# Optimization experiments

Measured on AMD Instinct MI355X. Metric: run time of the kernel, lower is better.

The kernel has to match this reference:

```python
import jax, jax.numpy as jnp
import numpy as np

CHAINS = [[15, 14, 13], [10, 11, 12], [5, 4, 3], [0, 1, 2]]
B, H, I = 2048, 1024, 3


def setup_inputs() -> dict:
    key = jax.random.key(0)
    ks = jax.random.split(key, 8)
    s = 1.0 / np.sqrt(H)
    return {
        "p3d": jax.random.normal(ks[0], (B, 16, I), dtype=jnp.float32),
        "Wih": jax.random.uniform(ks[1], (4 * H, I), jnp.float32, -s, s),
        "Whh": jax.random.uniform(ks[2], (4 * H, H), jnp.float32, -s, s),
        "bih": jax.random.uniform(ks[3], (4 * H,), jnp.float32, -s, s),
        "bhh": jax.random.uniform(ks[4], (4 * H,), jnp.float32, -s, s),
        "Wref": jax.random.uniform(ks[5], (I, H), jnp.float32, -s, s),
        "bref": jax.random.uniform(ks[6], (I,), jnp.float32, -s, s),
    }


def reference(p3d, Wih, Whh, bih, bhh, Wref, bref):
    # p3d: [B, 16, 3]; shared LSTMCell traverses the skeleton tree fwd+back.
    def cell(x, h, c):
        gates = x @ Wih.T + bih + h @ Whh.T + bhh  # [B, 4H]
        i, f, g, o = jnp.split(gates, 4, axis=-1)  # torch gate order i,f,g,o
        c2 = jax.nn.sigmoid(f) * c + jax.nn.sigmoid(i) * jnp.tanh(g)
        return jax.nn.sigmoid(o) * jnp.tanh(c2), c2

    z = jnp.zeros((p3d.shape[0], Whh.shape[1]), p3d.dtype)
    fh, fc = {}, {}
    # forward pass along limb chains (root of each chain starts from zeros)
    for chain in CHAINS:
        h, c = cell(p3d[:, chain[0]], z, z)
        fh[chain[0]], fc[chain[0]] = h, c
        for prev, cur in zip(chain[:-1], chain[1:]):
            h, c = cell(p3d[:, cur], fh[prev], fc[prev])
            fh[cur], fc[cur] = h, c
    # spine: merge hip ends (joints 2, 3) -> 6 -> 7
    hx, cx = (fh[2] + fh[3]) / 2, (fc[2] + fc[3]) / 2
    fh[6], fc[6] = cell(p3d[:, 6], hx, cx)
    fh[7], fc[7] = cell(p3d[:, 7], fh[6], fc[6])
    # merge neck + wrist ends (joints 7, 13, 12) -> 8 -> 9
    hx = (fh[7] + fh[13] + fh[12]) / 3
    cx = (fc[7] + fc[13] + fc[12]) / 3
    fh[8], fc[8] = cell(p3d[:, 8], hx, cx)
    fh[9], fc[9] = cell(p3d[:, 9], fh[8], fc[8])

    bh, bc = {}, {}
    bh[9], bc[9] = cell(p3d[:, 9], z, z)
    hx, cx = bh[9], bc[9]
    for i in [8, 7, 6]:
        hx, cx = cell(p3d[:, i], hx, cx)
        bh[i], bc[i] = hx, cx
    for chain in CHAINS:
        if chain[2] > 9:
            hx, cx = bh[8], bc[8]
        else:
            hx, cx = bh[6], bc[6]
        for i in reversed(chain):
            hx, cx = cell(p3d[:, i], hx, cx)
            bh[i], bc[i] = hx, cx

    FH = jnp.stack([fh[j] for j in range(16)], axis=1)  # [B, 16, H]
    BH = jnp.stack([bh[j] for j in range(16)], axis=1)  # [B, 16, H]
    out = (FH + BH) / 2.0
    return out @ Wref.T + bref  # [B, 16, 3]
```

## Files before the change

### kernel.cpp

```cpp
#include <hip/hip_runtime.h>
#include <cmath>

#define Bsz 2048
#define Hsz 1024
#define NG  4096
#define BM  256
#define BN  256
#define BK  64
#define NKT 16

typedef __attribute__((ext_vector_type(8))) short bf16x8;
typedef __attribute__((ext_vector_type(4))) float f32x4;

struct CellArgs {
  int ncells, b0;
  int joint[8];
  const short* hih[8];
  const float* cin[8];
  short* hoh[8];
  short* hol[8];
  float* cout[8];
};

struct ProjArgs {
  int ncells, b0;
  int joint[8];
  const short* hh[8];
  const short* hl[8];
};

__device__ __forceinline__ float sigmoidf_(float x) {
  return 1.0f / (1.0f + __expf(-x));
}
__device__ __forceinline__ float fast_tanh(float x) {
  float ax = fabsf(x);
  float e = __expf(2.0f * ax);
  float t = 1.0f - 2.0f / (e + 1.0f);
  return copysignf(t, x);
}
__device__ __forceinline__ float bf2f(short b) {
  unsigned u = ((unsigned)(unsigned short)b) << 16;
  float f; __builtin_memcpy(&f, &u, 4); return f;
}
__device__ __forceinline__ short f2bf(float f) {
  unsigned u; __builtin_memcpy(&u, &f, 4);
  u += 0x7fffu + ((u >> 16) & 1u);
  return (short)(u >> 16);
}
__device__ __forceinline__ void gl_lds16(const void* g, void* l) {
  __builtin_amdgcn_global_load_lds(
      (const __attribute__((address_space(1))) unsigned int*)g,
      (__attribute__((address_space(3))) unsigned int*)l, 16, 0, 0);
}

__launch_bounds__(512, 2)
__global__ void cell_kernel(const float* __restrict__ p3d,
                            const short* __restrict__ Whi,
                            const float4* __restrict__ wb,
                            CellArgs A) {
  __shared__ short Atile[2][BM * BK];
  __shared__ short Btile[2][BN * BK];
  __shared__ float xs[BM * 4];

  const int z = blockIdx.z;
  const short* __restrict__ hih = A.hih[z];
  const float* __restrict__ cin = A.cin[z];
  short* __restrict__ hoh = A.hoh[z];
  short* __restrict__ hol = A.hol[z];
  float* __restrict__ co  = A.cout[z];

  const int t = threadIdx.x;
  const int lane = t & 63;
  const int w = t >> 6;
  const int wm = w >> 2;
  const int wn = w & 3;
  const int m0 = blockIdx.x * BM;
  const int hc0 = blockIdx.y * 64;
  const int lc = lane & 15;
  const int kg = lane >> 4;
  const int xorv = lc & 7;

  const int l8 = lane >> 3, l7 = lane & 7;
  const int sSlot = (l7 ^ (l8 & 7)) * 8;
  int aOff[4], bOff[4];
  #pragma unroll
  for (int j = 0; j < 4; ++j) {
    const int chunk = j * 8 + w;
    aOff[j] = (m0 + chunk * 8 + l8) * Hsz + sSlot;
    const int np = chunk * 8 + l8;
    const int g = (np >> 4) & 3;
    const int hcl = ((np >> 6) << 4) + (np & 15);
    bOff[j] = (g * Hsz + hc0 + hcl) * Hsz + sSlot;
  }

  if (t < BM) {
    const float* p = p3d + ((size_t)(A.b0 + m0 + t) * 16 + A.joint[z]) * 3;
    xs[t * 4 + 0] = p[0];
    xs[t * 4 + 1] = p[1];
    xs[t * 4 + 2] = p[2];
  }
  __syncthreads();

  f32x4 acc[8][4];
  #pragma unroll
  for (int mf = 0; mf < 8; ++mf)
    #pragma unroll
    for (int nf = 0; nf < 4; ++nf) acc[mf][nf] = (f32x4){0.f, 0.f, 0.f, 0.f};

  const bool hasH = (hih != nullptr);

  auto stage = [&](int kt, int p) {
    const int k0 = kt * BK;
    #pragma unroll
    for (int j = 0; j < 4; ++j)
      gl_lds16(hih + aOff[j] + k0, &Atile[p][(j * 8 + w) * 512]);
    #pragma unroll
    for (int j = 0; j < 4; ++j)
      gl_lds16(Whi + bOff[j] + k0, &Btile[p][(j * 8 + w) * 512]);
  };

  if (hasH) {
    stage(0, 0);
    stage(1, 1);
    asm volatile("s_waitcnt vmcnt(8)" ::: "memory");
    __builtin_amdgcn_s_barrier();

    for (int kt = 0; kt < NKT; ++kt) {
      const int p = kt & 1;
      const short* Ab = &Atile[p][0];
      const short* Bb = &Btile[p][0];
      #pragma unroll
      for (int ks = 0; ks < 2; ++ks) {
        bf16x8 af[8], bf[4];
        #pragma unroll
        for (int mf = 0; mf < 8; ++mf) {
          const int r = wm * 128 + mf * 16 + lc;
          af[mf] = *(const bf16x8*)(Ab + r * 64 + (((ks * 4 + kg) ^ xorv) * 8));
        }
        #pragma unroll
        for (int nf = 0; nf < 4; ++nf) {
          const int np = wn * 64 + nf * 16 + lc;
          bf[nf] = *(const bf16x8*)(Bb + np * 64 + (((ks * 4 + kg) ^ xorv) * 8));
        }
        __builtin_amdgcn_s_setprio(1);
        #pragma unroll
        for (int mf = 0; mf < 8; ++mf)
          #pragma unroll
          for (int nf = 0; nf < 4; ++nf)
            acc[mf][nf] = __builtin_amdgcn_mfma_f32_16x16x32_bf16(
                af[mf], bf[nf], acc[mf][nf], 0, 0, 0);
        __builtin_amdgcn_s_setprio(0);
      }
      asm volatile("s_waitcnt lgkmcnt(0)" ::: "memory");
      __builtin_amdgcn_s_barrier();
      if (kt + 2 < NKT) {
        stage(kt + 2, p);
        asm volatile("s_waitcnt vmcnt(8)" ::: "memory");
      } else {
        asm volatile("s_waitcnt vmcnt(0)" ::: "memory");
      }
      __builtin_amdgcn_s_barrier();
    }
  }

  const int hc = hc0 + wn * 16 + lc;
  float4 wv[4];
  #pragma unroll
  for (int g = 0; g < 4; ++g) wv[g] = wb[g * Hsz + hc];
  #pragma unroll
  for (int mf = 0; mf < 8; ++mf) {
    #pragma unroll
    for (int r = 0; r < 4; ++r) {
      const int ml = wm * 128 + mf * 16 + kg * 4 + r;
      const int m = m0 + ml;
      const float x0 = xs[ml * 4 + 0], x1 = xs[ml * 4 + 1], x2 = xs[ml * 4 + 2];
      float pre[4];
      #pragma unroll
      for (int g = 0; g < 4; ++g)
        pre[g] = acc[mf][g][r] + wv[g].w + x0 * wv[g].x + x1 * wv[g].y + x2 * wv[g].z;
      const float ci = cin ? cin[(size_t)m * Hsz + hc] : 0.0f;
      const float c2 = sigmoidf_(pre[1]) * ci + sigmoidf_(pre[0]) * fast_tanh(pre[2]);
      const float h2 = sigmoidf_(pre[3]) * fast_tanh(c2);
      co[(size_t)m * Hsz + hc] = c2;
      const short hhi = f2bf(h2);
      hoh[(size_t)m * Hsz + hc] = hhi;
      hol[(size_t)m * Hsz + hc] = f2bf(h2 - bf2f(hhi));
    }
  }
}

__global__ void prep_kernel(const float* __restrict__ Whh,
                            const float* __restrict__ Wih,
                            const float* __restrict__ bih,
                            const float* __restrict__ bhh,
                            short* __restrict__ Whi,
                            float4* __restrict__ wb) {
  const int n4 = NG * Hsz / 4;
  int i = blockIdx.x * blockDim.x + threadIdx.x;
  for (; i < n4; i += gridDim.x * blockDim.x) {
    float4 wv = reinterpret_cast<const float4*>(Whh)[i];
    short4 hi;
    hi.x = f2bf(wv.x);
    hi.y = f2bf(wv.y);
    hi.z = f2bf(wv.z);
    hi.w = f2bf(wv.w);
    reinterpret_cast<short4*>(Whi)[i] = hi;
  }
  int c = blockIdx.x * blockDim.x + threadIdx.x;
  if (c < NG)
    wb[c] = make_float4(Wih[c * 3], Wih[c * 3 + 1], Wih[c * 3 + 2],
                        bih[c] + bhh[c]);
}

__global__ void merge_kernel(short* __restrict__ ohh, short* __restrict__ ohl,
                             float* __restrict__ oc,
                             const short* __restrict__ ahh, const short* __restrict__ ahl,
                             const float* __restrict__ ac,
                             const short* __restrict__ bhh, const short* __restrict__ bhl,
                             const float* __restrict__ bc,
                             const short* __restrict__ chh, const short* __restrict__ chl,
                             const float* __restrict__ cc,
                             float scale, int n4) {
  int i = blockIdx.x * blockDim.x + threadIdx.x;
  for (; i < n4; i += gridDim.x * blockDim.x) {
    short4 ah = reinterpret_cast<const short4*>(ahh)[i];
    short4 al = reinterpret_cast<const short4*>(ahl)[i];
    short4 bh = reinterpret_cast<const short4*>(bhh)[i];
    short4 bl = reinterpret_cast<const short4*>(bhl)[i];
    float h[4];
    h[0] = bf2f(ah.x) + bf2f(al.x) + bf2f(bh.x) + bf2f(bl.x);
    h[1] = bf2f(ah.y) + bf2f(al.y) + bf2f(bh.y) + bf2f(bl.y);
    h[2] = bf2f(ah.z) + bf2f(al.z) + bf2f(bh.z) + bf2f(bl.z);
    h[3] = bf2f(ah.w) + bf2f(al.w) + bf2f(bh.w) + bf2f(bl.w);
    float4 c = reinterpret_cast<const float4*>(ac)[i];
    float4 c2 = reinterpret_cast<const float4*>(bc)[i];
    c.x += c2.x; c.y += c2.y; c.z += c2.z; c.w += c2.w;
    if (chh != nullptr) {
      short4 ch = reinterpret_cast<const short4*>(chh)[i];
      short4 cl = reinterpret_cast<const short4*>(chl)[i];
      h[0] += bf2f(ch.x) + bf2f(cl.x);
      h[1] += bf2f(ch.y) + bf2f(cl.y);
      h[2] += bf2f(ch.z) + bf2f(cl.z);
      h[3] += bf2f(ch.w) + bf2f(cl.w);
      float4 c3 = reinterpret_cast<const float4*>(cc)[i];
      c.x += c3.x; c.y += c3.y; c.z += c3.z; c.w += c3.w;
    }
    short4 hi, lo;
    float v;
    v = h[0] * scale; hi.x = f2bf(v); lo.x = f2bf(v - bf2f(hi.x));
    v = h[1] * scale; hi.y = f2bf(v); lo.y = f2bf(v - bf2f(hi.y));
    v = h[2] * scale; hi.z = f2bf(v); lo.z = f2bf(v - bf2f(hi.z));
    v = h[3] * scale; hi.w = f2bf(v); lo.w = f2bf(v - bf2f(hi.w));
    reinterpret_cast<short4*>(ohh)[i] = hi;
    reinterpret_cast<short4*>(ohl)[i] = lo;
    c.x *= scale; c.y *= scale; c.z *= scale; c.w *= scale;
    reinterpret_cast<float4*>(oc)[i] = c;
  }
}

__global__ void init_out_kernel(float* __restrict__ out, const float* __restrict__ bref) {
  int i = blockIdx.x * blockDim.x + threadIdx.x;
  const int n = Bsz * 16 * 3;
  for (; i < n; i += gridDim.x * blockDim.x) out[i] = bref[i % 3];
}

__global__ void proj_kernel(ProjArgs P, const float* __restrict__ Wref,
                            float* __restrict__ out) {
  const int cell = blockIdx.x;
  const int b = blockIdx.y;
  const int t = threadIdx.x;
  const short4* hh = reinterpret_cast<const short4*>(P.hh[cell] + (size_t)b * Hsz);
  const short4* hl = reinterpret_cast<const short4*>(P.hl[cell] + (size_t)b * Hsz);
  const float4* W0 = reinterpret_cast<const float4*>(Wref);
  const float4* W1 = reinterpret_cast<const float4*>(Wref + Hsz);
  const float4* W2 = reinterpret_cast<const float4*>(Wref + 2 * Hsz);
  short4 a = hh[t], l = hl[t];
  float v0 = 0.5f * (bf2f(a.x) + bf2f(l.x));
  float v1 = 0.5f * (bf2f(a.y) + bf2f(l.y));
  float v2 = 0.5f * (bf2f(a.z) + bf2f(l.z));
  float v3 = 0.5f * (bf2f(a.w) + bf2f(l.w));
  float4 w0 = W0[t], w1 = W1[t], w2 = W2[t];
  float s0 = v0 * w0.x + v1 * w0.y + v2 * w0.z + v3 * w0.w;
  float s1 = v0 * w1.x + v1 * w1.y + v2 * w1.z + v3 * w1.w;
  float s2 = v0 * w2.x + v1 * w2.y + v2 * w2.z + v3 * w2.w;
  #pragma unroll
  for (int off = 32; off > 0; off >>= 1) {
    s0 += __shfl_down(s0, off);
    s1 += __shfl_down(s1, off);
    s2 += __shfl_down(s2, off);
  }
  __shared__ float red[4][3];
  const int wave = t >> 6;
  if ((t & 63) == 0) { red[wave][0] = s0; red[wave][1] = s1; red[wave][2] = s2; }
  __syncthreads();
  if (t == 0) {
    float r0 = red[0][0] + red[1][0] + red[2][0] + red[3][0];
    float r1 = red[0][1] + red[1][1] + red[2][1] + red[3][1];
    float r2 = red[0][2] + red[1][2] + red[2][2] + red[3][2];
    float* o = out + ((size_t)(P.b0 + b) * 16 + P.joint[cell]) * 3;
    atomicAdd(o + 0, r0);
    atomicAdd(o + 1, r1);
    atomicAdd(o + 2, r2);
  }
}

extern "C" void kernel_launch(void* const* d_in, const int* in_sizes, int n_in,
                              void* d_out, int out_size, void* d_ws, size_t ws_size,
                              hipStream_t stream) {
  const float* p3d  = (const float*)d_in[0];
  const float* Wih  = (const float*)d_in[1];
  const float* Whh  = (const float*)d_in[2];
  const float* bih  = (const float*)d_in[3];
  const float* bhh  = (const float*)d_in[4];
  const float* Wref = (const float*)d_in[5];
  const float* bref = (const float*)d_in[6];
  float* out = (float*)d_out;

  char* ws = (char*)d_ws;
  short* Whi = (short*)ws;
  float4* wb = (float4*)(Whi + (size_t)NG * Hsz);
  char* pool = (char*)(wb + NG);
  const size_t fixed = (size_t)(pool - ws);

  int chunkB = Bsz;
  while (chunkB > BM && fixed + (size_t)12 * chunkB * Hsz * 8 > ws_size)
    chunkB >>= 1;
  const size_t CH = (size_t)chunkB * Hsz;
  auto SH = [&](int s) { return (short*)(pool + (size_t)s * CH * 8); };
  auto SL = [&](int s) { return SH(s) + CH; };
  auto SC = [&](int s) { return (float*)(SL(s) + CH); };

  const dim3 blk(256);
  prep_kernel<<<dim3(4096), blk, 0, stream>>>(Whh, Wih, bih, bhh, Whi, wb);
  init_out_kernel<<<dim3(96), blk, 0, stream>>>(out, bref);

  for (int b0 = 0; b0 < Bsz; b0 += chunkB) {
    auto run_cells = [&](CellArgs& A) {
      A.b0 = b0;
      dim3 grid(chunkB / BM, Hsz / 64, A.ncells);
      cell_kernel<<<grid, dim3(512), 0, stream>>>(p3d, Whi, wb, A);
    };
    auto run_proj = [&](ProjArgs& P) {
      P.b0 = b0;
      proj_kernel<<<dim3(P.ncells, chunkB), blk, 0, stream>>>(P, Wref, out);
    };
    auto cellset = [&](CellArgs& A, int i, int joint, int sin, int sout) {
      A.joint[i] = joint;
      if (sin >= 0) { A.hih[i] = SH(sin); A.cin[i] = SC(sin); }
      else          { A.hih[i] = nullptr; A.cin[i] = nullptr; }
      A.hoh[i] = SH(sout); A.hol[i] = SL(sout); A.cout[i] = SC(sout);
    };
    auto projset = [&](ProjArgs& P, int i, int joint, int s) {
      P.joint[i] = joint; P.hh[i] = SH(s); P.hl[i] = SL(s);
    };
    auto domerge = [&](int dst, int s1, int s2, int s3, float scale) {
      merge_kernel<<<dim3(1024), blk, 0, stream>>>(
          SH(dst), SL(dst), SC(dst), SH(s1), SL(s1), SC(s1),
          SH(s2), SL(s2), SC(s2),
          s3 >= 0 ? SH(s3) : nullptr, s3 >= 0 ? SL(s3) : nullptr,
          s3 >= 0 ? SC(s3) : nullptr, scale, (int)(CH / 4));
    };

    {
      CellArgs A{}; A.ncells = 5;
      cellset(A, 0, 15, -1, 0); cellset(A, 1, 10, -1, 1); cellset(A, 2, 5, -1, 2);
      cellset(A, 3,  0, -1, 3); cellset(A, 4,  9, -1, 4);
      run_cells(A);
      ProjArgs P{}; P.ncells = 5;
      projset(P, 0, 15, 0); projset(P, 1, 10, 1); projset(P, 2, 5, 2);
      projset(P, 3,  0, 3); projset(P, 4,  9, 4);
      run_proj(P);
    }
    {
      CellArgs A{}; A.ncells = 5;
      cellset(A, 0, 14, 0, 5); cellset(A, 1, 11, 1, 6); cellset(A, 2, 4, 2, 7);
      cellset(A, 3,  1, 3, 8); cellset(A, 4,  8, 4, 9);
      run_cells(A);
      ProjArgs P{}; P.ncells = 5;
      projset(P, 0, 14, 5); projset(P, 1, 11, 6); projset(P, 2, 4, 7);
      projset(P, 3,  1, 8); projset(P, 4,  8, 9);
      run_proj(P);
    }
    {
      CellArgs A{}; A.ncells = 7;
      cellset(A, 0, 13, 5, 0);  cellset(A, 1, 12, 6, 1);  cellset(A, 2, 3, 7, 2);
      cellset(A, 3,  2, 8, 3);  cellset(A, 4,  7, 9, 4);  cellset(A, 5, 13, 9, 10);
      cellset(A, 6, 12, 9, 11);
      run_cells(A);
      ProjArgs P{}; P.ncells = 7;
      projset(P, 0, 13, 0);  projset(P, 1, 12, 1);  projset(P, 2, 3, 2);
      projset(P, 3,  2, 3);  projset(P, 4,  7, 4);  projset(P, 5, 13, 10);
      projset(P, 6, 12, 11);
      run_proj(P);
    }
    domerge(5, 3, 2, -1, 0.5f);
    {
      CellArgs A{}; A.ncells = 4;
      cellset(A, 0,  6, 5, 6);  cellset(A, 1,  6, 4, 7);
      cellset(A, 2, 14, 10, 8); cellset(A, 3, 11, 11, 9);
      run_cells(A);
      ProjArgs P{}; P.ncells = 4;
      projset(P, 0, 6, 6); projset(P, 1, 6, 7); projset(P, 2, 14, 8);
      projset(P, 3, 11, 9);
      run_proj(P);
    }
    {
      CellArgs A{}; A.ncells = 5;
      cellset(A, 0,  7, 6, 4);  cellset(A, 1, 15, 8, 5);  cellset(A, 2, 10, 9, 10);
      cellset(A, 3,  3, 7, 11); cellset(A, 4,  2, 7, 2);
      run_cells(A);
      ProjArgs P{}; P.ncells = 5;
      projset(P, 0, 7, 4);  projset(P, 1, 15, 5); projset(P, 2, 10, 10);
      projset(P, 3, 3, 11); projset(P, 4,  2, 2);
      run_proj(P);
    }
    domerge(6, 4, 0, 1, 1.0f / 3.0f);
    {
      CellArgs A{}; A.ncells = 3;
      cellset(A, 0, 8, 6, 0); cellset(A, 1, 4, 11, 1); cellset(A, 2, 1, 2, 3);
      run_cells(A);
      ProjArgs P{}; P.ncells = 3;
      projset(P, 0, 8, 0); projset(P, 1, 4, 1); projset(P, 2, 1, 3);
      run_proj(P);
    }
    {
      CellArgs A{}; A.ncells = 3;
      cellset(A, 0, 9, 0, 2); cellset(A, 1, 5, 1, 4); cellset(A, 2, 0, 3, 5);
      run_cells(A);
      ProjArgs P{}; P.ncells = 3;
      projset(P, 0, 9, 2); projset(P, 1, 5, 4); projset(P, 2, 0, 5);
      run_proj(P);
    }
  }
}
```

Before: 952.2 us.

## Fuse output projection into LSTM cell epilogue and drop bf16 low-part hidden state

The Wref projection is computed inside the cell kernel epilogue with shuffle reductions, an LDS partial-sum buffer and atomics, which removes the separate proj_kernel launches. The hidden state is now stored only as a single bf16 value instead of a hi/lo bf16 pair, which cuts hidden-state write and read traffic and workspace size. Cells whose outputs are never consumed skip their h and c stores. The trade-off is lower precision in the recurrent hidden state and in the projection input, plus some extra epilogue work per GEMM tile.

```diff
diff --git a/kernel.cpp b/kernel.cpp
--- a/kernel.cpp
+++ b/kernel.cpp
@@ -5,7 +5,6 @@
 #define Hsz 1024
 #define NG  4096
 #define BM  256
-#define BN  256
 #define BK  64
 #define NKT 16
 
@@ -18,15 +17,7 @@
   const short* hih[8];
   const float* cin[8];
   short* hoh[8];
-  short* hol[8];
   float* cout[8];
-};
-
-struct ProjArgs {
-  int ncells, b0;
-  int joint[8];
-  const short* hh[8];
-  const short* hl[8];
 };
 
 __device__ __forceinline__ float sigmoidf_(float x) {
@@ -57,17 +48,20 @@
 __global__ void cell_kernel(const float* __restrict__ p3d,
                             const short* __restrict__ Whi,
                             const float4* __restrict__ wb,
+                            const float* __restrict__ Wref,
+                            float* __restrict__ out,
                             CellArgs A) {
   __shared__ short Atile[2][BM * BK];
-  __shared__ short Btile[2][BN * BK];
+  __shared__ short Btile[2][BM * BK];
   __shared__ float xs[BM * 4];
+  __shared__ float psum[4][BM][3];
 
   const int z = blockIdx.z;
   const short* __restrict__ hih = A.hih[z];
   const float* __restrict__ cin = A.cin[z];
   short* __restrict__ hoh = A.hoh[z];
-  short* __restrict__ hol = A.hol[z];
   float* __restrict__ co  = A.cout[z];
+  const int joint = A.joint[z];
 
   const int t = threadIdx.x;
   const int lane = t & 63;
@@ -94,7 +88,7 @@
   }
 
   if (t < BM) {
-    const float* p = p3d + ((size_t)(A.b0 + m0 + t) * 16 + A.joint[z]) * 3;
+    const float* p = p3d + ((size_t)(A.b0 + m0 + t) * 16 + joint) * 3;
     xs[t * 4 + 0] = p[0];
     xs[t * 4 + 1] = p[1];
     xs[t * 4 + 2] = p[2];
@@ -167,6 +161,10 @@
   float4 wv[4];
   #pragma unroll
   for (int g = 0; g < 4; ++g) wv[g] = wb[g * Hsz + hc];
+  const float wr0 = 0.5f * Wref[hc];
+  const float wr1 = 0.5f * Wref[Hsz + hc];
+  const float wr2 = 0.5f * Wref[2 * Hsz + hc];
+  const bool doStore = (hoh != nullptr);
   #pragma unroll
   for (int mf = 0; mf < 8; ++mf) {
     #pragma unroll
@@ -181,11 +179,33 @@
       const float ci = cin ? cin[(size_t)m * Hsz + hc] : 0.0f;
       const float c2 = sigmoidf_(pre[1]) * ci + sigmoidf_(pre[0]) * fast_tanh(pre[2]);
       const float h2 = sigmoidf_(pre[3]) * fast_tanh(c2);
-      co[(size_t)m * Hsz + hc] = c2;
-      const short hhi = f2bf(h2);
-      hoh[(size_t)m * Hsz + hc] = hhi;
-      hol[(size_t)m * Hsz + hc] = f2bf(h2 - bf2f(hhi));
-    }
+      if (doStore) {
+        co[(size_t)m * Hsz + hc] = c2;
+        hoh[(size_t)m * Hsz + hc] = f2bf(h2);
+      }
+      float s0 = h2 * wr0, s1 = h2 * wr1, s2 = h2 * wr2;
+      s0 += __shfl_xor(s0, 1); s0 += __shfl_xor(s0, 2);
+      s0 += __shfl_xor(s0, 4); s0 += __shfl_xor(s0, 8);
+      s1 += __shfl_xor(s1, 1); s1 += __shfl_xor(s1, 2);
+      s1 += __shfl_xor(s1, 4); s1 += __shfl_xor(s1, 8);
+      s2 += __shfl_xor(s2, 1); s2 += __shfl_xor(s2, 2);
+      s2 += __shfl_xor(s2, 4); s2 += __shfl_xor(s2, 8);
+      if (lc == 0) {
+        psum[wn][ml][0] = s0;
+        psum[wn][ml][1] = s1;
+        psum[wn][ml][2] = s2;
+      }
+    }
+  }
+  __syncthreads();
+  if (t < BM) {
+    const float r0 = psum[0][t][0] + psum[1][t][0] + psum[2][t][0] + psum[3][t][0];
+    const float r1 = psum[0][t][1] + psum[1][t][1] + psum[2][t][1] + psum[3][t][1];
+    const float r2 = psum[0][t][2] + psum[1][t][2] + psum[2][t][2] + psum[3][t][2];
+    float* o = out + ((size_t)(A.b0 + m0 + t) * 16 + joint) * 3;
+    atomicAdd(o + 0, r0);
+    atomicAdd(o + 1, r1);
+    atomicAdd(o + 2, r2);
   }
 }
 
@@ -212,47 +232,36 @@
                         bih[c] + bhh[c]);
 }
 
-__global__ void merge_kernel(short* __restrict__ ohh, short* __restrict__ ohl,
-                             float* __restrict__ oc,
-                             const short* __restrict__ ahh, const short* __restrict__ ahl,
-                             const float* __restrict__ ac,
-                             const short* __restrict__ bhh, const short* __restrict__ bhl,
-                             const float* __restrict__ bc,
-                             const short* __restrict__ chh, const short* __restrict__ chl,
-                             const float* __restrict__ cc,
+__global__ void merge_kernel(short* __restrict__ ohh, float* __restrict__ oc,
+                             const short* __restrict__ ahh, const float* __restrict__ ac,
+                             const short* __restrict__ bhh, const float* __restrict__ bc,
+                             const short* __restrict__ chh, const float* __restrict__ cc,
                              float scale, int n4) {
   int i = blockIdx.x * blockDim.x + threadIdx.x;
   for (; i < n4; i += gridDim.x * blockDim.x) {
     short4 ah = reinterpret_cast<const short4*>(ahh)[i];
-    short4 al = reinterpret_cast<const short4*>(ahl)[i];
     short4 bh = reinterpret_cast<const short4*>(bhh)[i];
-    short4 bl = reinterpret_cast<const short4*>(bhl)[i];
     float h[4];
-    h[0] = bf2f(ah.x) + bf2f(al.x) + bf2f(bh.x) + bf2f(bl.x);
-    h[1] = bf2f(ah.y) + bf2f(al.y) + bf2f(bh.y) + bf2f(bl.y);
-    h[2] = bf2f(ah.z) + bf2f(al.z) + bf2f(bh.z) + bf2f(bl.z);
-    h[3] = bf2f(ah.w) + bf2f(al.w) + bf2f(bh.w) + bf2f(bl.w);
+    h[0] = bf2f(ah.x) + bf2f(bh.x);
+    h[1] = bf2f(ah.y) + bf2f(bh.y);
+    h[2] = bf2f(ah.z) + bf2f(bh.z);
+    h[3] = bf2f(ah.w) + bf2f(bh.w);
     float4 c = reinterpret_cast<const float4*>(ac)[i];
     float4 c2 = reinterpret_cast<const float4*>(bc)[i];
     c.x += c2.x; c.y += c2.y; c.z += c2.z; c.w += c2.w;
     if (chh != nullptr) {
       short4 ch = reinterpret_cast<const short4*>(chh)[i];
-      short4 cl = reinterpret_cast<const short4*>(chl)[i];
-      h[0] += bf2f(ch.x) + bf2f(cl.x);
-      h[1] += bf2f(ch.y) + bf2f(cl.y);
-      h[2] += bf2f(ch.z) + bf2f(cl.z);
-      h[3] += bf2f(ch.w) + bf2f(cl.w);
+      h[0] += bf2f(ch.x); h[1] += bf2f(ch.y);
+      h[2] += bf2f(ch.z); h[3] += bf2f(ch.w);
       float4 c3 = reinterpret_cast<const float4*>(cc)[i];
       c.x += c3.x; c.y += c3.y; c.z += c3.z; c.w += c3.w;
     }
-    short4 hi, lo;
-    float v;
-    v = h[0] * scale; hi.x = f2bf(v); lo.x = f2bf(v - bf2f(hi.x));
-    v = h[1] * scale; hi.y = f2bf(v); lo.y = f2bf(v - bf2f(hi.y));
-    v = h[2] * scale; hi.z = f2bf(v); lo.z = f2bf(v - bf2f(hi.z));
-    v = h[3] * scale; hi.w = f2bf(v); lo.w = f2bf(v - bf2f(hi.w));
+    short4 hi;
+    hi.x = f2bf(h[0] * scale);
+    hi.y = f2bf(h[1] * scale);
+    hi.z = f2bf(h[2] * scale);
+    hi.w = f2bf(h[3] * scale);
     reinterpret_cast<short4*>(ohh)[i] = hi;
-    reinterpret_cast<short4*>(ohl)[i] = lo;
     c.x *= scale; c.y *= scale; c.z *= scale; c.w *= scale;
     reinterpret_cast<float4*>(oc)[i] = c;
   }
@@ -262,46 +271,6 @@
   int i = blockIdx.x * blockDim.x + threadIdx.x;
   const int n = Bsz * 16 * 3;
   for (; i < n; i += gridDim.x * blockDim.x) out[i] = bref[i % 3];
-}
-
-__global__ void proj_kernel(ProjArgs P, const float* __restrict__ Wref,
-                            float* __restrict__ out) {
-  const int cell = blockIdx.x;
-  const int b = blockIdx.y;
-  const int t = threadIdx.x;
-  const short4* hh = reinterpret_cast<const short4*>(P.hh[cell] + (size_t)b * Hsz);
-  const short4* hl = reinterpret_cast<const short4*>(P.hl[cell] + (size_t)b * Hsz);
-  const float4* W0 = reinterpret_cast<const float4*>(Wref);
-  const float4* W1 = reinterpret_cast<const float4*>(Wref + Hsz);
-  const float4* W2 = reinterpret_cast<const float4*>(Wref + 2 * Hsz);
-  short4 a = hh[t], l = hl[t];
-  float v0 = 0.5f * (bf2f(a.x) + bf2f(l.x));
-  float v1 = 0.5f * (bf2f(a.y) + bf2f(l.y));
-  float v2 = 0.5f * (bf2f(a.z) + bf2f(l.z));
-  float v3 = 0.5f * (bf2f(a.w) + bf2f(l.w));
-  float4 w0 = W0[t], w1 = W1[t], w2 = W2[t];
-  float s0 = v0 * w0.x + v1 * w0.y + v2 * w0.z + v3 * w0.w;
-  float s1 = v0 * w1.x + v1 * w1.y + v2 * w1.z + v3 * w1.w;
-  float s2 = v0 * w2.x + v1 * w2.y + v2 * w2.z + v3 * w2.w;
-  #pragma unroll
-  for (int off = 32; off > 0; off >>= 1) {
-    s0 += __shfl_down(s0, off);
-    s1 += __shfl_down(s1, off);
-    s2 += __shfl_down(s2, off);
-  }
-  __shared__ float red[4][3];
-  const int wave = t >> 6;
-  if ((t & 63) == 0) { red[wave][0] = s0; red[wave][1] = s1; red[wave][2] = s2; }
-  __syncthreads();
-  if (t == 0) {
-    float r0 = red[0][0] + red[1][0] + red[2][0] + red[3][0];
-    float r1 = red[0][1] + red[1][1] + red[2][1] + red[3][1];
-    float r2 = red[0][2] + red[1][2] + red[2][2] + red[3][2];
-    float* o = out + ((size_t)(P.b0 + b) * 16 + P.joint[cell]) * 3;
-    atomicAdd(o + 0, r0);
-    atomicAdd(o + 1, r1);
-    atomicAdd(o + 2, r2);
-  }
 }
 
 extern "C" void kernel_launch(void* const* d_in, const int* in_sizes, int n_in,
@@ -323,12 +292,11 @@
   const size_t fixed = (size_t)(pool - ws);
 
   int chunkB = Bsz;
-  while (chunkB > BM && fixed + (size_t)12 * chunkB * Hsz * 8 > ws_size)
+  while (chunkB > BM && fixed + (size_t)12 * chunkB * Hsz * 6 > ws_size)
     chunkB >>= 1;
   const size_t CH = (size_t)chunkB * Hsz;
-  auto SH = [&](int s) { return (short*)(pool + (size_t)s * CH * 8); };
-  auto SL = [&](int s) { return SH(s) + CH; };
-  auto SC = [&](int s) { return (float*)(SL(s) + CH); };
+  auto SH = [&](int s) { return (short*)(pool + (size_t)s * CH * 6); };
+  auto SC = [&](int s) { return (float*)(pool + (size_t)s * CH * 6 + CH * 2); };
 
   const dim3 blk(256);
   prep_kernel<<<dim3(4096), blk, 0, stream>>>(Whh, Wih, bih, bhh, Whi, wb);
@@ -338,98 +306,70 @@
     auto run_cells = [&](CellArgs& A) {
       A.b0 = b0;
       dim3 grid(chunkB / BM, Hsz / 64, A.ncells);
-      cell_kernel<<<grid, dim3(512), 0, stream>>>(p3d, Whi, wb, A);
+      cell_kernel<<<grid, dim3(512), 0, stream>>>(p3d, Whi, wb, Wref, out, A);
     };
-    auto run_proj = [&](ProjArgs& P) {
-      P.b0 = b0;
-      proj_kernel<<<dim3(P.ncells, chunkB), blk, 0, stream>>>(P, Wref, out);
-    };
-    auto cellset = [&](CellArgs& A, int i, int joint, int sin, int sout) {
+    auto cellset = [&](CellArgs& A, int i, int joint, int sin, int sout, bool store) {
       A.joint[i] = joint;
       if (sin >= 0) { A.hih[i] = SH(sin); A.cin[i] = SC(sin); }
       else          { A.hih[i] = nullptr; A.cin[i] = nullptr; }
-      A.hoh[i] = SH(sout); A.hol[i] = SL(sout); A.cout[i] = SC(sout);
-    };
-    auto projset = [&](ProjArgs& P, int i, int joint, int s) {
-      P.joint[i] = joint; P.hh[i] = SH(s); P.hl[i] = SL(s);
+      if (store) { A.hoh[i] = SH(sout); A.cout[i] = SC(sout); }
+      else       { A.hoh[i] = nullptr;  A.cout[i] = nullptr; }
     };
     auto domerge = [&](int dst, int s1, int s2, int s3, float scale) {
       merge_kernel<<<dim3(1024), blk, 0, stream>>>(
-          SH(dst), SL(dst), SC(dst), SH(s1), SL(s1), SC(s1),
-          SH(s2), SL(s2), SC(s2),
-          s3 >= 0 ? SH(s3) : nullptr, s3 >= 0 ? SL(s3) : nullptr,
-          s3 >= 0 ? SC(s3) : nullptr, scale, (int)(CH / 4));
+          SH(dst), SC(dst), SH(s1), SC(s1), SH(s2), SC(s2),
+          s3 >= 0 ? SH(s3) : nullptr, s3 >= 0 ? SC(s3) : nullptr,
+          scale, (int)(CH / 4));
     };
 
     {
       CellArgs A{}; A.ncells = 5;
-      cellset(A, 0, 15, -1, 0); cellset(A, 1, 10, -1, 1); cellset(A, 2, 5, -1, 2);
-      cellset(A, 3,  0, -1, 3); cellset(A, 4,  9, -1, 4);
-      run_cells(A);
-      ProjArgs P{}; P.ncells = 5;
-      projset(P, 0, 15, 0); projset(P, 1, 10, 1); projset(P, 2, 5, 2);
-      projset(P, 3,  0, 3); projset(P, 4,  9, 4);
-      run_proj(P);
+      cellset(A, 0, 15, -1, 0, true); cellset(A, 1, 10, -1, 1, true);
+      cellset(A, 2,  5, -1, 2, true); cellset(A, 3,  0, -1, 3, true);
+      cellset(A, 4,  9, -1, 4, true);
+      run_cells(A);
     }
     {
       CellArgs A{}; A.ncells = 5;
-      cellset(A, 0, 14, 0, 5); cellset(A, 1, 11, 1, 6); cellset(A, 2, 4, 2, 7);
-      cellset(A, 3,  1, 3, 8); cellset(A, 4,  8, 4, 9);
-      run_cells(A);
-      ProjArgs P{}; P.ncells = 5;
-      projset(P, 0, 14, 5); projset(P, 1, 11, 6); projset(P, 2, 4, 7);
-      projset(P, 3,  1, 8); projset(P, 4,  8, 9);
-      run_proj(P);
+      cellset(A, 0, 14, 0, 5, true); cellset(A, 1, 11, 1, 6, true);
+      cellset(A, 2,  4, 2, 7, true); cellset(A, 3,  1, 3, 8, true);
+      cellset(A, 4,  8, 4, 9, true);
+      run_cells(A);
     }
     {
       CellArgs A{}; A.ncells = 7;
-      cellset(A, 0, 13, 5, 0);  cellset(A, 1, 12, 6, 1);  cellset(A, 2, 3, 7, 2);
-      cellset(A, 3,  2, 8, 3);  cellset(A, 4,  7, 9, 4);  cellset(A, 5, 13, 9, 10);
-      cellset(A, 6, 12, 9, 11);
-      run_cells(A);
-      ProjArgs P{}; P.ncells = 7;
-      projset(P, 0, 13, 0);  projset(P, 1, 12, 1);  projset(P, 2, 3, 2);
-      projset(P, 3,  2, 3);  projset(P, 4,  7, 4);  projset(P, 5, 13, 10);
-      projset(P, 6, 12, 11);
-      run_proj(P);
+      cellset(A, 0, 13, 5, 0, true);  cellset(A, 1, 12, 6, 1, true);
+      cellset(A, 2,  3, 7, 2, true);  cellset(A, 3,  2, 8, 3, true);
+      cellset(A, 4,  7, 9, 4, true);  cellset(A, 5, 13, 9, 10, true);
+      cellset(A, 6, 12, 9, 11, true);
+      run_cells(A);
     }
     domerge(5, 3, 2, -1, 0.5f);
     {
       CellArgs A{}; A.ncells = 4;
-      cellset(A, 0,  6, 5, 6);  cellset(A, 1,  6, 4, 7);
-      cellset(A, 2, 14, 10, 8); cellset(A, 3, 11, 11, 9);
-      run_cells(A);
-      ProjArgs P{}; P.ncells = 4;
-      projset(P, 0, 6, 6); projset(P, 1, 6, 7); projset(P, 2, 14, 8);
-      projset(P, 3, 11, 9);
-      run_proj(P);
+      cellset(A, 0,  6, 5, 6, true);  cellset(A, 1,  6, 4, 7, true);
+      cellset(A, 2, 14, 10, 8, true); cellset(A, 3, 11, 11, 9, true);
+      run_cells(A);
     }
     {
       CellArgs A{}; A.ncells = 5;
-      cellset(A, 0,  7, 6, 4);  cellset(A, 1, 15, 8, 5);  cellset(A, 2, 10, 9, 10);
-      cellset(A, 3,  3, 7, 11); cellset(A, 4,  2, 7, 2);
-      run_cells(A);
-      ProjArgs P{}; P.ncells = 5;
-      projset(P, 0, 7, 4);  projset(P, 1, 15, 5); projset(P, 2, 10, 10);
-      projset(P, 3, 3, 11); projset(P, 4,  2, 2);
-      run_proj(P);
+      cellset(A, 0,  7, 6, 4, true);   cellset(A, 1, 15, 8, 5, false);
+      cellset(A, 2, 10, 9, 10, false); cellset(A, 3,  3, 7, 11, true);
+      cellset(A, 4,  2, 7, 2, true);
+      run_cells(A);
     }
     domerge(6, 4, 0, 1, 1.0f / 3.0f);
     {
       CellArgs A{}; A.ncells = 3;
-      cellset(A, 0, 8, 6, 0); cellset(A, 1, 4, 11, 1); cellset(A, 2, 1, 2, 3);
-      run_cells(A);
-      ProjArgs P{}; P.ncells = 3;
-      projset(P, 0, 8, 0); projset(P, 1, 4, 1); projset(P, 2, 1, 3);
-      run_proj(P);
+      cellset(A, 0, 8, 6, 0, true); cellset(A, 1, 4, 11, 1, true);
+      cellset(A, 2, 1, 2, 3, true);
+      run_cells(A);
     }
     {
       CellArgs A{}; A.ncells = 3;
-      cellset(A, 0, 9, 0, 2); cellset(A, 1, 5, 1, 4); cellset(A, 2, 0, 3, 5);
-      run_cells(A);
-      ProjArgs P{}; P.ncells = 3;
-      projset(P, 0, 9, 2); projset(P, 1, 5, 4); projset(P, 2, 0, 5);
-      run_proj(P);
-    }
-  }
-}
+      cellset(A, 0, 9, 0, 2, false); cellset(A, 1, 5, 1, 4, false);
+      cellset(A, 2, 0, 3, 5, false);
+      run_cells(A);
+    }
+  }
+}
```

New measurement: 1.159 ms. 1.22x slower.
